# Optimization experiments

Hardware: AMD Instinct MI355X
Metric: run time of the kernel (lower is better)

Reference implementation:

```python
import jax, jax.numpy as jnp
import numpy as np

EPS = 1e-6

def poincare_pairwise_distance(x, c):
    """x: (B,N,E) points in Poincare ball, c: (C,E) centroids. Returns (B,N,C)."""
    x2 = jnp.sum(x * x, axis=-1)                  # (B,N)
    c2 = jnp.sum(c * c, axis=-1)                  # (C,)
    xc = jnp.einsum('bne,ce->bnc', x, c)          # (B,N,C)
    sq = jnp.maximum(x2[..., None] + c2[None, None, :] - 2.0 * xc, 0.0)  # ||x-c||^2
    den = (1.0 - x2)[..., None] * (1.0 - c2)[None, None, :]
    arg = 1.0 + 2.0 * sq / jnp.maximum(den, EPS)
    return jnp.arccosh(jnp.maximum(arg, 1.0 + EPS))

def setup_inputs() -> dict:
    key = jax.random.key(0)
    k1, k2 = jax.random.split(key)
    B, N, E, C = 32, 4096, 64, 256
    # scale so points lie strictly inside the unit ball (valid hyperbolic coords)
    node_repr = jax.random.normal(k1, (B, N, E), dtype=jnp.float32) * 0.05
    mask = jnp.ones((B, N, 1), dtype=jnp.float32)
    centroid = jax.random.normal(k2, (C, E), dtype=jnp.float32) * 0.01
    return {"node_repr": node_repr, "mask": mask, "centroid": centroid}

def reference(node_repr, mask, centroid):
    dist = poincare_pairwise_distance(node_repr, centroid)   # (B,N,C)
    dist = dist * mask                                       # mask: (B,N,1) broadcasts
    graph_dist = jnp.sum(dist, axis=1) / jnp.sum(mask, axis=1)  # (B,C)
    return graph_dist, dist
```

## Files before the change

### kernel.cpp

```cpp
#include <hip/hip_runtime.h>
#include <math.h>

#define E_DIM 64
#define C_DIM 256
#define EPS_F 1e-6f
#define LN2_F 0.69314718056f

typedef __attribute__((ext_vector_type(8))) short short8;
typedef __attribute__((ext_vector_type(4))) float f32x4;

__device__ __forceinline__ unsigned short f2bf(float f) {
    unsigned int u = __float_as_uint(f);
    u += 0x7FFFu + ((u >> 16) & 1u);
    return (unsigned short)(u >> 16);
}

__device__ __forceinline__ short8 pack8(float4 a, float4 b) {
    short8 h;
    h[0] = (short)f2bf(a.x); h[1] = (short)f2bf(a.y);
    h[2] = (short)f2bf(a.z); h[3] = (short)f2bf(a.w);
    h[4] = (short)f2bf(b.x); h[5] = (short)f2bf(b.y);
    h[6] = (short)f2bf(b.z); h[7] = (short)f2bf(b.w);
    return h;
}

#define WS_F    0
#define WS_C2   32768
#define WS_RD2  33792
#define WS_INVM 34816

__global__ __launch_bounds__(C_DIM) void cdist_pre(
    const float* __restrict__ cent,
    const float* __restrict__ mask,
    unsigned char* __restrict__ ws,
    int N)
{
    const int t = threadIdx.x;
    if (blockIdx.x == 0) {
        float r[E_DIM];
        const float* cr = cent + t * E_DIM;
        #pragma unroll
        for (int e = 0; e < E_DIM; e += 4) {
            float4 v = *reinterpret_cast<const float4*>(cr + e);
            r[e] = v.x; r[e+1] = v.y; r[e+2] = v.z; r[e+3] = v.w;
        }
        float c2 = 0.f;
        #pragma unroll
        for (int e = 0; e < E_DIM; ++e) c2 = fmaf(r[e], r[e], c2);
        ((float*)(ws + WS_C2))[t]  = c2;
        ((float*)(ws + WS_RD2))[t] = 2.f / (1.f - c2);

        const int ct16 = t >> 4, l15 = t & 15;
        short8* F = (short8*)(ws + WS_F);
        #pragma unroll
        for (int kf = 0; kf < 2; ++kf) {
            #pragma unroll
            for (int q = 0; q < 4; ++q) {
                short8 h;
                #pragma unroll
                for (int j = 0; j < 8; ++j)
                    h[j] = (short)f2bf(r[kf * 32 + q * 8 + j]);
                F[(ct16 * 2 + kf) * 64 + 16 * q + l15] = h;
            }
        }
    } else {
        const int b = blockIdx.x - 1;
        float s = 0.f;
        for (int n = t; n < N; n += C_DIM) s += mask[(size_t)b * N + n];
        #pragma unroll
        for (int off = 32; off > 0; off >>= 1) s += __shfl_down(s, off, 64);
        __shared__ float partial[4];
        if ((t & 63) == 0) partial[t >> 6] = s;
        __syncthreads();
        if (t == 0) {
            float tot = partial[0] + partial[1] + partial[2] + partial[3];
            ((float*)(ws + WS_INVM))[b] = 1.f / tot;
        }
    }
}

__global__ __launch_bounds__(256) void cdist_mfma(
    const float* __restrict__ x,
    const float* __restrict__ mask,
    const unsigned char* __restrict__ ws,
    float*       __restrict__ graph_acc,
    float*       __restrict__ dist,
    int N)
{
    const int tid  = threadIdx.x;
    const int w    = tid >> 6;
    const int lane = tid & 63;
    const int l15  = lane & 15;
    const int q    = lane >> 4;
    const int n0   = blockIdx.x * 64;
    const int b    = blockIdx.y;

    const short8* F   = (const short8*)(ws + WS_F);
    const float*  c2w = (const float*)(ws + WS_C2);
    const float*  rd2w= (const float*)(ws + WS_RD2);

    short8 bfrag[4][2];
    #pragma unroll
    for (int ct = 0; ct < 4; ++ct)
        #pragma unroll
        for (int kf = 0; kf < 2; ++kf)
            bfrag[ct][kf] = F[((w * 4 + ct) * 2 + kf) * 64 + lane];

    float c2v[4], rd2v[4], gsum[4];
    #pragma unroll
    for (int ct = 0; ct < 4; ++ct) {
        const int c = w * 64 + ct * 16 + l15;
        c2v[ct] = c2w[c]; rd2v[ct] = rd2w[c]; gsum[ct] = 0.f;
    }

    const size_t rowbase = (size_t)b * N + n0;

    #pragma unroll
    for (int rt = 0; rt < 4; ++rt) {
        const size_t row = rowbase + rt * 16 + l15;
        const float* xr = x + row * E_DIM + q * 8;
        float4 v0 = *reinterpret_cast<const float4*>(xr);
        float4 v1 = *reinterpret_cast<const float4*>(xr + 4);
        float4 v2 = *reinterpret_cast<const float4*>(xr + 32);
        float4 v3 = *reinterpret_cast<const float4*>(xr + 36);

        float ss = 0.f;
        ss = fmaf(v0.x, v0.x, ss); ss = fmaf(v0.y, v0.y, ss);
        ss = fmaf(v0.z, v0.z, ss); ss = fmaf(v0.w, v0.w, ss);
        ss = fmaf(v1.x, v1.x, ss); ss = fmaf(v1.y, v1.y, ss);
        ss = fmaf(v1.z, v1.z, ss); ss = fmaf(v1.w, v1.w, ss);
        ss = fmaf(v2.x, v2.x, ss); ss = fmaf(v2.y, v2.y, ss);
        ss = fmaf(v2.z, v2.z, ss); ss = fmaf(v2.w, v2.w, ss);
        ss = fmaf(v3.x, v3.x, ss); ss = fmaf(v3.y, v3.y, ss);
        ss = fmaf(v3.z, v3.z, ss); ss = fmaf(v3.w, v3.w, ss);
        ss += __shfl_xor(ss, 16);
        ss += __shfl_xor(ss, 32);

        const float rbrow = __builtin_amdgcn_rcpf(1.f - ss);
        const float krow  = LN2_F * mask[row];

        short8 a0 = pack8(v0, v1);
        short8 a1 = pack8(v2, v3);

        f32x4 acc[4];
        #pragma unroll
        for (int ct = 0; ct < 4; ++ct) {
            f32x4 z = {0.f, 0.f, 0.f, 0.f};
            z = __builtin_amdgcn_mfma_f32_16x16x32_bf16(a0, bfrag[ct][0], z, 0, 0, 0);
            z = __builtin_amdgcn_mfma_f32_16x16x32_bf16(a1, bfrag[ct][1], z, 0, 0, 0);
            acc[ct] = z;
        }

        float ar[4], rbr[4], kr[4];
        #pragma unroll
        for (int reg = 0; reg < 4; ++reg) {
            const int src = q * 4 + reg;
            ar[reg]  = __shfl(ss,    src);
            rbr[reg] = __shfl(rbrow, src);
            kr[reg]  = __shfl(krow,  src);
        }
        #pragma unroll
        for (int ct = 0; ct < 4; ++ct) {
            const int c = w * 64 + ct * 16 + l15;
            #pragma unroll
            for (int reg = 0; reg < 4; ++reg) {
                const float dot = acc[ct][reg];
                float sq = fmaf(-2.f, dot, ar[reg] + c2v[ct]);
                sq = fmaxf(sq, 0.f);
                float u = fmaxf(sq * (rbr[reg] * rd2v[ct]), EPS_F);
                float t = u + __builtin_amdgcn_sqrtf(fmaf(u, u, u + u));
                const float d = __builtin_amdgcn_logf(1.f + t) * kr[reg];
                dist[(rowbase + rt * 16 + q * 4 + reg) * C_DIM + c] = d;
                gsum[ct] += d;
            }
        }
    }

    const float inv = ((const float*)(ws + WS_INVM))[b];
    #pragma unroll
    for (int ct = 0; ct < 4; ++ct) {
        float s = gsum[ct];
        s += __shfl_xor(s, 16);
        s += __shfl_xor(s, 32);
        if (q == 0)
            atomicAdd(&graph_acc[b * C_DIM + w * 64 + ct * 16 + l15], s * inv);
    }
}

extern "C" void kernel_launch(void* const* d_in, const int* in_sizes, int n_in,
                              void* d_out, int out_size, void* d_ws, size_t ws_size,
                              hipStream_t stream) {
    const float* x    = (const float*)d_in[0];
    const float* mask = (const float*)d_in[1];
    const float* cent = (const float*)d_in[2];
    float* out = (float*)d_out;

    const long long BN = in_sizes[1];
    const int E = in_sizes[0] / (int)BN;
    const int C = in_sizes[2] / E;
    const int B = (int)(((long long)out_size - BN * C) / C);
    const int N = (int)(BN / B);

    float* graph_acc = out;
    float* dist_out  = out + (size_t)B * C;
    unsigned char* ws = (unsigned char*)d_ws;

    hipMemsetAsync(graph_acc, 0, (size_t)B * C * sizeof(float), stream);

    cdist_pre<<<dim3(B + 1), C_DIM, 0, stream>>>(cent, mask, ws, N);
    cdist_mfma<<<dim3(N / 64, B), 256, 0, stream>>>(x, mask, ws, graph_acc, dist_out, N);
}
```

Baseline: 191.4 us.

## Stage dist tiles through LDS for float4 stores and prefetch next row tile

Each wave now writes its 16x64 distance tile into a padded per-wave shared-memory buffer and then reads it back as float4s, so global stores become 16-byte vector writes with each row contiguous instead of scattered 4-byte stores. The row loop is no longer unrolled, and the x and mask loads for the next 16-row tile are issued before the current tile's math to hide load latency. Launch bounds now request 4 blocks per CU to cap register use. No barrier is used between the LDS write and read, which relies on wave-local ordering, and the extra LDS traffic and reduced unrolling may eat into the gain.

Measured after the change: 180.2 us. -5.8%, faster.

```diff
diff --git a/kernel.cpp b/kernel.cpp
--- a/kernel.cpp
+++ b/kernel.cpp
@@ -5,6 +5,7 @@
 #define C_DIM 256
 #define EPS_F 1e-6f
 #define LN2_F 0.69314718056f
+#define TP    68
 
 typedef __attribute__((ext_vector_type(8))) short short8;
 typedef __attribute__((ext_vector_type(4))) float f32x4;
@@ -79,7 +80,7 @@
     }
 }
 
-__global__ __launch_bounds__(256) void cdist_mfma(
+__global__ __launch_bounds__(256, 4) void cdist_mfma(
     const float* __restrict__ x,
     const float* __restrict__ mask,
     const unsigned char* __restrict__ ws,
@@ -95,9 +96,11 @@
     const int n0   = blockIdx.x * 64;
     const int b    = blockIdx.y;
 
-    const short8* F   = (const short8*)(ws + WS_F);
-    const float*  c2w = (const float*)(ws + WS_C2);
-    const float*  rd2w= (const float*)(ws + WS_RD2);
+    __shared__ __align__(16) float sT[4][16 * TP];
+
+    const short8* F    = (const short8*)(ws + WS_F);
+    const float*  c2w  = (const float*)(ws + WS_C2);
+    const float*  rd2w = (const float*)(ws + WS_RD2);
 
     short8 bfrag[4][2];
     #pragma unroll
@@ -114,33 +117,46 @@
     }
 
     const size_t rowbase = (size_t)b * N + n0;
-
-    #pragma unroll
+    float* sW = sT[w];
+
+    const float* xr0 = x + (rowbase + l15) * E_DIM + q * 8;
+    float4 v0 = *reinterpret_cast<const float4*>(xr0);
+    float4 v1 = *reinterpret_cast<const float4*>(xr0 + 4);
+    float4 v2 = *reinterpret_cast<const float4*>(xr0 + 32);
+    float4 v3 = *reinterpret_cast<const float4*>(xr0 + 36);
+    float  mk = mask[rowbase + l15];
+
+    #pragma unroll 1
     for (int rt = 0; rt < 4; ++rt) {
-        const size_t row = rowbase + rt * 16 + l15;
-        const float* xr = x + row * E_DIM + q * 8;
-        float4 v0 = *reinterpret_cast<const float4*>(xr);
-        float4 v1 = *reinterpret_cast<const float4*>(xr + 4);
-        float4 v2 = *reinterpret_cast<const float4*>(xr + 32);
-        float4 v3 = *reinterpret_cast<const float4*>(xr + 36);
+        float4 u0 = v0, u1 = v1, u2 = v2, u3 = v3;
+        float  mkc = mk;
+
+        if (rt < 3) {
+            const float* xr = x + (rowbase + (rt + 1) * 16 + l15) * E_DIM + q * 8;
+            v0 = *reinterpret_cast<const float4*>(xr);
+            v1 = *reinterpret_cast<const float4*>(xr + 4);
+            v2 = *reinterpret_cast<const float4*>(xr + 32);
+            v3 = *reinterpret_cast<const float4*>(xr + 36);
+            mk = mask[rowbase + (rt + 1) * 16 + l15];
+        }
 
         float ss = 0.f;
-        ss = fmaf(v0.x, v0.x, ss); ss = fmaf(v0.y, v0.y, ss);
-        ss = fmaf(v0.z, v0.z, ss); ss = fmaf(v0.w, v0.w, ss);
-        ss = fmaf(v1.x, v1.x, ss); ss = fmaf(v1.y, v1.y, ss);
-        ss = fmaf(v1.z, v1.z, ss); ss = fmaf(v1.w, v1.w, ss);
-        ss = fmaf(v2.x, v2.x, ss); ss = fmaf(v2.y, v2.y, ss);
-        ss = fmaf(v2.z, v2.z, ss); ss = fmaf(v2.w, v2.w, ss);
-        ss = fmaf(v3.x, v3.x, ss); ss = fmaf(v3.y, v3.y, ss);
-        ss = fmaf(v3.z, v3.z, ss); ss = fmaf(v3.w, v3.w, ss);
+        ss = fmaf(u0.x, u0.x, ss); ss = fmaf(u0.y, u0.y, ss);
+        ss = fmaf(u0.z, u0.z, ss); ss = fmaf(u0.w, u0.w, ss);
+        ss = fmaf(u1.x, u1.x, ss); ss = fmaf(u1.y, u1.y, ss);
+        ss = fmaf(u1.z, u1.z, ss); ss = fmaf(u1.w, u1.w, ss);
+        ss = fmaf(u2.x, u2.x, ss); ss = fmaf(u2.y, u2.y, ss);
+        ss = fmaf(u2.z, u2.z, ss); ss = fmaf(u2.w, u2.w, ss);
+        ss = fmaf(u3.x, u3.x, ss); ss = fmaf(u3.y, u3.y, ss);
+        ss = fmaf(u3.z, u3.z, ss); ss = fmaf(u3.w, u3.w, ss);
         ss += __shfl_xor(ss, 16);
         ss += __shfl_xor(ss, 32);
 
         const float rbrow = __builtin_amdgcn_rcpf(1.f - ss);
-        const float krow  = LN2_F * mask[row];
-
-        short8 a0 = pack8(v0, v1);
-        short8 a1 = pack8(v2, v3);
+        const float krow  = LN2_F * mkc;
+
+        short8 a0 = pack8(u0, u1);
+        short8 a1 = pack8(u2, u3);
 
         f32x4 acc[4];
         #pragma unroll
@@ -159,20 +175,29 @@
             rbr[reg] = __shfl(rbrow, src);
             kr[reg]  = __shfl(krow,  src);
         }
+
         #pragma unroll
         for (int ct = 0; ct < 4; ++ct) {
-            const int c = w * 64 + ct * 16 + l15;
             #pragma unroll
             for (int reg = 0; reg < 4; ++reg) {
                 const float dot = acc[ct][reg];
                 float sq = fmaf(-2.f, dot, ar[reg] + c2v[ct]);
                 sq = fmaxf(sq, 0.f);
-                float u = fmaxf(sq * (rbr[reg] * rd2v[ct]), EPS_F);
-                float t = u + __builtin_amdgcn_sqrtf(fmaf(u, u, u + u));
+                float uu = fmaxf(sq * (rbr[reg] * rd2v[ct]), EPS_F);
+                float t  = uu + __builtin_amdgcn_sqrtf(fmaf(uu, uu, uu + uu));
                 const float d = __builtin_amdgcn_logf(1.f + t) * kr[reg];
-                dist[(rowbase + rt * 16 + q * 4 + reg) * C_DIM + c] = d;
+                sW[(q * 4 + reg) * TP + ct * 16 + l15] = d;
                 gsum[ct] += d;
             }
+        }
+
+        #pragma unroll
+        for (int i = 0; i < 4; ++i) {
+            const int row2 = i * 4 + (lane >> 4);
+            const int col2 = (lane & 15) * 4;
+            float4 val = *reinterpret_cast<const float4*>(&sW[row2 * TP + col2]);
+            *reinterpret_cast<float4*>(
+                dist + (rowbase + rt * 16 + row2) * C_DIM + w * 64 + col2) = val;
         }
     }
 
```
